# Performance work log

Hardware: AMD Instinct MI355X
Metric: run time of the kernel (lower is better)

Reference implementation:

```python
import jax, jax.numpy as jnp
import numpy as np

EPS = 1e-05


def setup_inputs() -> dict:
    key = jax.random.key(0)
    k1, _ = jax.random.split(key)
    x = jax.random.normal(k1, (4, 8192, 1024), dtype=jnp.float32)
    weight = jnp.ones((1024,), dtype=jnp.float32)
    return {"x": x, "weight": weight}


def reference(x, weight):
    # GMRNorm, elementwise=True path. The original computes, per channel c,
    # mean[b,t,c] = sum_{s<=t} x[b,s,c] / (t+1) via a [T,T] triangular matmul,
    # with the (0,0) entry zeroed so mean at t=0 is 0. This is exactly a
    # cumulative sum divided by the prefix count, computed here in O(B*T*C).
    x = x.astype(jnp.float32)
    B, T, C = x.shape
    counts = jnp.arange(1, T + 1, dtype=jnp.float32)[:, None]  # [T,1]
    mean = jnp.cumsum(x, axis=1) / counts                      # [B,T,C]
    mean = mean.at[:, 0, :].set(0.0)                           # causal_matrix[0,0] = 0
    xc = x - mean
    norm_x = jnp.mean(xc * xc, axis=-1, keepdims=True)         # per-timestep variance over C
    x_normed = xc * jax.lax.rsqrt(norm_x + EPS)
    return weight * x_normed
```

## Files before the change

### kernel.cpp

```cpp
#include <hip/hip_runtime.h>

#define T_    8192
#define C_    1024
#define TCH   16
#define NCH   (T_ / TCH)
#define CPB   4
#define ROWS  (CPB * TCH)
#define NSB   (T_ / ROWS)
#define BATCH 4

typedef float v4f __attribute__((ext_vector_type(4)));

__global__ __launch_bounds__(256) void k_sums(const float* __restrict__ x,
                                              float* __restrict__ Scs,
                                              float* __restrict__ agg) {
    const int sb = blockIdx.x;
    const int b  = blockIdx.y;
    const int c4 = threadIdx.x * 4;
    const float* xp = x + ((size_t)(b * T_ + sb * ROWS)) * C_ + c4;
    float* Sp = Scs + ((size_t)(b * NCH + sb * CPB)) * C_ + c4;

    float4 tot = make_float4(0.f, 0.f, 0.f, 0.f);
#pragma unroll
    for (int j = 0; j < CPB; ++j) {
        float4 cs = make_float4(0.f, 0.f, 0.f, 0.f);
#pragma unroll
        for (int i = 0; i < TCH; ++i) {
            float4 v = *(const float4*)(xp + (size_t)(j * TCH + i) * C_);
            cs.x += v.x; cs.y += v.y; cs.z += v.z; cs.w += v.w;
        }
        *(float4*)(Sp + (size_t)j * C_) = cs;
        tot.x += cs.x; tot.y += cs.y; tot.z += cs.z; tot.w += cs.w;
    }
    *(float4*)(agg + ((size_t)(b * NSB + sb)) * C_ + c4) = tot;
}

__global__ __launch_bounds__(256) void k_norm(const float* __restrict__ x,
                                              const float* __restrict__ Scs,
                                              const float* __restrict__ agg,
                                              const float* __restrict__ w,
                                              float* __restrict__ out) {
    const int sb  = blockIdx.x;
    const int b   = blockIdx.y;
    const int tid = threadIdx.x;
    const int c4  = tid * 4;

    __shared__ float pre2[C_];

    float4 excl = make_float4(0.f, 0.f, 0.f, 0.f);
    const float* ap = agg + (size_t)b * NSB * C_ + c4;
#pragma unroll 4
    for (int j = 0; j < sb; ++j) {
        float4 v = *(const float4*)(ap + (size_t)j * C_);
        excl.x += v.x; excl.y += v.y; excl.z += v.z; excl.w += v.w;
    }
    *(float4*)&pre2[c4] = excl;
    __syncthreads();

    const int wave = tid >> 6;
    const int lane = tid & 63;
    const int ch   = sb * CPB + wave;
    const int cb   = lane * 4;
    const float* Sp = Scs + ((size_t)(b * NCH + sb * CPB)) * C_;

    float4 racc[4], wt[4];
#pragma unroll
    for (int q = 0; q < 4; ++q) {
        float4 p2 = *(const float4*)&pre2[q * 256 + cb];
        racc[q] = p2;
        for (int j = 0; j < wave; ++j) {
            float4 s = *(const float4*)(Sp + (size_t)j * C_ + q * 256 + cb);
            racc[q].x += s.x; racc[q].y += s.y; racc[q].z += s.z; racc[q].w += s.w;
        }
        wt[q] = *(const float4*)(w + q * 256 + cb);
    }

    const int t0 = ch * TCH;
    const float* xq = x   + (size_t)(b * T_ + t0) * C_;
    float*       op = out + (size_t)(b * T_ + t0) * C_;
    const float invC = 1.0f / (float)C_;

#pragma unroll
    for (int h = 0; h < TCH / BATCH; ++h) {
        float4 xc[BATCH][4];
        float  sq[BATCH];

#pragma unroll
        for (int i = 0; i < BATCH; ++i) {
            const int tt = t0 + h * BATCH + i;
            const float m = (tt == 0) ? 0.0f
                                      : __builtin_amdgcn_rcpf((float)(tt + 1));
            float s = 0.f;
#pragma unroll
            for (int q = 0; q < 4; ++q) {
                float4 v = *(const float4*)(xq + (size_t)(h * BATCH + i) * C_
                                               + q * 256 + cb);
                racc[q].x += v.x; float a0 = v.x - racc[q].x * m; s += a0 * a0;
                racc[q].y += v.y; float a1 = v.y - racc[q].y * m; s += a1 * a1;
                racc[q].z += v.z; float a2 = v.z - racc[q].z * m; s += a2 * a2;
                racc[q].w += v.w; float a3 = v.w - racc[q].w * m; s += a3 * a3;
                xc[i][q] = make_float4(a0, a1, a2, a3);
            }
            sq[i] = s;
        }

#pragma unroll
        for (int off = 32; off; off >>= 1) {
#pragma unroll
            for (int i = 0; i < BATCH; ++i)
                sq[i] += __shfl_xor(sq[i], off, 64);
        }

        float scale[BATCH];
#pragma unroll
        for (int i = 0; i < BATCH; ++i)
            scale[i] = __builtin_amdgcn_rsqf(sq[i] * invC + 1e-5f);

#pragma unroll
        for (int i = 0; i < BATCH; ++i) {
#pragma unroll
            for (int q = 0; q < 4; ++q) {
                v4f o;
                o.x = wt[q].x * xc[i][q].x * scale[i];
                o.y = wt[q].y * xc[i][q].y * scale[i];
                o.z = wt[q].z * xc[i][q].z * scale[i];
                o.w = wt[q].w * xc[i][q].w * scale[i];
                __builtin_nontemporal_store(o,
                    (v4f*)(op + (size_t)(h * BATCH + i) * C_ + q * 256 + cb));
            }
        }
    }
}

extern "C" void kernel_launch(void* const* d_in, const int* in_sizes, int n_in,
                              void* d_out, int out_size, void* d_ws, size_t ws_size,
                              hipStream_t stream) {
    const float* x = (const float*)d_in[0];
    const float* w = (const float*)d_in[1];
    float* out = (float*)d_out;

    const int B = in_sizes[0] / (T_ * C_);

    float* Scs = (float*)d_ws;
    float* agg = Scs + (size_t)B * NCH * C_;

    dim3 g(NSB, B);
    k_sums<<<g, 256, 0, stream>>>(x, Scs, agg);
    k_norm<<<g, 256, 0, stream>>>(x, Scs, agg, w, out);
}
```

Before: 257.8 us.

## Shrink chunk size and decouple norm-kernel grid from sums-kernel superblocks

Chunks shrink from 16 to 8 rows, and the normalization kernel now runs over 32-row blocks (two per 64-row superblock), so it launches twice as many blocks, each wave handling 8 rows. The aim is more parallelism and shorter serial per-wave work in k_norm, with launch bounds hinting 4 blocks per CU. In exchange, the redundant exclusive prefix over the agg rows is read by twice as many blocks. The intra-superblock prefix loop can also run longer, up to 7 chunk sums per wave.

```diff
diff --git a/kernel.cpp b/kernel.cpp
--- a/kernel.cpp
+++ b/kernel.cpp
@@ -2,11 +2,13 @@
 
 #define T_    8192
 #define C_    1024
-#define TCH   16
+#define TCH   8
 #define NCH   (T_ / TCH)
-#define CPB   4
-#define ROWS  (CPB * TCH)
-#define NSB   (T_ / ROWS)
+#define SBR   64
+#define NSB   (T_ / SBR)
+#define CPB   (SBR / TCH)
+#define K2R   32
+#define NK2   (T_ / K2R)
 #define BATCH 4
 
 typedef float v4f __attribute__((ext_vector_type(4)));
@@ -17,7 +19,7 @@
     const int sb = blockIdx.x;
     const int b  = blockIdx.y;
     const int c4 = threadIdx.x * 4;
-    const float* xp = x + ((size_t)(b * T_ + sb * ROWS)) * C_ + c4;
+    const float* xp = x + ((size_t)(b * T_ + sb * SBR)) * C_ + c4;
     float* Sp = Scs + ((size_t)(b * NCH + sb * CPB)) * C_ + c4;
 
     float4 tot = make_float4(0.f, 0.f, 0.f, 0.f);
@@ -35,47 +37,51 @@
     *(float4*)(agg + ((size_t)(b * NSB + sb)) * C_ + c4) = tot;
 }
 
-__global__ __launch_bounds__(256) void k_norm(const float* __restrict__ x,
-                                              const float* __restrict__ Scs,
-                                              const float* __restrict__ agg,
-                                              const float* __restrict__ w,
-                                              float* __restrict__ out) {
-    const int sb  = blockIdx.x;
+__global__ __launch_bounds__(256, 4) void k_norm(const float* __restrict__ x,
+                                                 const float* __restrict__ Scs,
+                                                 const float* __restrict__ agg,
+                                                 const float* __restrict__ w,
+                                                 float* __restrict__ out) {
+    const int blk = blockIdx.x;
     const int b   = blockIdx.y;
     const int tid = threadIdx.x;
     const int c4  = tid * 4;
 
     __shared__ float pre2[C_];
 
+    const int sb2 = blk >> 1;
     float4 excl = make_float4(0.f, 0.f, 0.f, 0.f);
     const float* ap = agg + (size_t)b * NSB * C_ + c4;
 #pragma unroll 4
-    for (int j = 0; j < sb; ++j) {
+    for (int j = 0; j < sb2; ++j) {
         float4 v = *(const float4*)(ap + (size_t)j * C_);
         excl.x += v.x; excl.y += v.y; excl.z += v.z; excl.w += v.w;
     }
     *(float4*)&pre2[c4] = excl;
     __syncthreads();
 
-    const int wave = tid >> 6;
-    const int lane = tid & 63;
-    const int ch   = sb * CPB + wave;
-    const int cb   = lane * 4;
-    const float* Sp = Scs + ((size_t)(b * NCH + sb * CPB)) * C_;
+    const int wave   = tid >> 6;
+    const int lane   = tid & 63;
+    const int cb     = lane * 4;
+    const int chunkg = blk * (K2R / TCH) + wave;
+    const int intra  = chunkg & (CPB - 1);
+    const float* Ssb = Scs + ((size_t)b * NCH + (size_t)(chunkg & ~(CPB - 1))) * C_;
 
     float4 racc[4], wt[4];
 #pragma unroll
     for (int q = 0; q < 4; ++q) {
-        float4 p2 = *(const float4*)&pre2[q * 256 + cb];
-        racc[q] = p2;
-        for (int j = 0; j < wave; ++j) {
-            float4 s = *(const float4*)(Sp + (size_t)j * C_ + q * 256 + cb);
+        racc[q] = *(const float4*)&pre2[q * 256 + cb];
+        wt[q]   = *(const float4*)(w + q * 256 + cb);
+    }
+    for (int j = 0; j < intra; ++j) {
+#pragma unroll
+        for (int q = 0; q < 4; ++q) {
+            float4 s = *(const float4*)(Ssb + (size_t)j * C_ + q * 256 + cb);
             racc[q].x += s.x; racc[q].y += s.y; racc[q].z += s.z; racc[q].w += s.w;
         }
-        wt[q] = *(const float4*)(w + q * 256 + cb);
     }
 
-    const int t0 = ch * TCH;
+    const int t0 = chunkg * TCH;
     const float* xq = x   + (size_t)(b * T_ + t0) * C_;
     float*       op = out + (size_t)(b * T_ + t0) * C_;
     const float invC = 1.0f / (float)C_;
@@ -144,7 +150,9 @@
     float* Scs = (float*)d_ws;
     float* agg = Scs + (size_t)B * NCH * C_;
 
-    dim3 g(NSB, B);
-    k_sums<<<g, 256, 0, stream>>>(x, Scs, agg);
-    k_norm<<<g, 256, 0, stream>>>(x, Scs, agg, w, out);
+    dim3 g1(NSB, B);
+    k_sums<<<g1, 256, 0, stream>>>(x, Scs, agg);
+
+    dim3 g2(NK2, B);
+    k_norm<<<g2, 256, 0, stream>>>(x, Scs, agg, w, out);
 }
```

After: 262.5 us. About the same (+1.8%).
